# Performance work log

Measured on AMD Instinct MI355X. Metric: run time of the kernel, lower is better.

The kernel has to match this reference:

```python
import jax, jax.numpy as jnp
import numpy as np

DIM = 128
CODEBOOK_SIZE = 1024


def setup_inputs() -> dict:
    key = jax.random.key(0)
    kx, ke = jax.random.split(key)
    x = jax.random.normal(kx, (16, 4096, DIM), dtype=jnp.float32)
    # kaiming_uniform_ on (codebook_size, dim): bound = sqrt(6 / fan_in), fan_in = dim
    bound = float(np.sqrt(6.0 / DIM))
    embed = jax.random.uniform(ke, (CODEBOOK_SIZE, DIM), dtype=jnp.float32,
                               minval=-bound, maxval=bound)
    return {"x": x, "embed": embed}


def reference(x, embed):
    orig_shape = x.shape
    flat = x.reshape(-1, x.shape[-1])                     # [N, D]
    x2 = jnp.sum(flat * flat, axis=1, keepdims=True)      # [N, 1]
    e2 = jnp.sum(embed * embed, axis=1)                   # [K]
    dist = -(x2 - 2.0 * (flat @ embed.T) + e2[None, :])   # [N, K]
    embed_ind = jnp.argmax(dist, axis=-1)                 # [N]
    embed_ind = embed_ind.reshape(orig_shape[:-1])        # [B, S]
    quantize = jnp.take(embed, embed_ind, axis=0)         # [B, S, D]
    return quantize, embed_ind
```

## Files before the change

### kernel.cpp

```cpp
#include <hip/hip_runtime.h>

#define DIM     128
#define NCODES  1024
#define TILE_M  64
#define LDSS    136
#define DELTA   0.02f
#define RPB     4
#define RGRID   1024

typedef __attribute__((ext_vector_type(8))) _Float16 half8;
typedef __attribute__((ext_vector_type(4))) _Float16 half4;
typedef __attribute__((ext_vector_type(4))) float    f32x4;


__global__ __launch_bounds__(256) void prep_kernel(
    const float* __restrict__ embed, double* __restrict__ e2d,
    float* __restrict__ e2f, _Float16* __restrict__ eh, int* __restrict__ cnt)
{
  if (blockIdx.x == 0 && threadIdx.x == 0) *cnt = 0;
  const int w = threadIdx.x >> 6;
  const int l = threadIdx.x & 63;
  const int c = blockIdx.x * 4 + w;
  const float* row = embed + (size_t)c * DIM;
  float v0 = row[l], v1 = row[l + 64];
  eh[(size_t)c * DIM + l]      = (_Float16)v0;
  eh[(size_t)c * DIM + 64 + l] = (_Float16)v1;
  double sq = (double)v0 * v0 + (double)v1 * v1;
  #pragma unroll
  for (int off = 32; off >= 1; off >>= 1) sq += __shfl_down(sq, off, 64);
  if (l == 0) { e2d[c] = sq; e2f[c] = (float)sq; }
}

__global__ __launch_bounds__(256) void transpose_kernel(
    const float* __restrict__ embed, float* __restrict__ embedT)
{
  __shared__ float tile[64][65];
  const int c0 = blockIdx.y * 64;
  const int k0 = blockIdx.x * 64;
  const int t = threadIdx.x;
  #pragma unroll
  for (int i = 0; i < 16; ++i) {
    int idx = t + i * 256;
    int r = idx >> 6, c = idx & 63;
    tile[r][c] = embed[(size_t)(c0 + r) * DIM + k0 + c];
  }
  __syncthreads();
  #pragma unroll
  for (int i = 0; i < 16; ++i) {
    int idx = t + i * 256;
    int r = idx >> 6, c = idx & 63;
    embedT[(size_t)(k0 + r) * NCODES + c0 + c] = tile[c][r];
  }
}

__global__ __launch_bounds__(256, 2) void pass1_kernel(
    const float* __restrict__ x, const float* __restrict__ embed,
    const _Float16* __restrict__ eh, const float* __restrict__ e2f,
    float* __restrict__ outQ, float* __restrict__ outIdx,
    int* __restrict__ cnt, int* __restrict__ list)
{
  __shared__ _Float16 xh[TILE_M * LDSS];
  __shared__ float rb_best[4][TILE_M];
  __shared__ float rb_sec [4][TILE_M];
  __shared__ int   rb_idx [4][TILE_M];
  __shared__ int   fidx[TILE_M];

  const int tid  = threadIdx.x;
  const int row0 = blockIdx.x * TILE_M;

  {
    const f32x4* x4 = (const f32x4*)(x + (size_t)row0 * DIM);
    #pragma unroll
    for (int i = 0; i < 8; ++i) {
      int e = tid + i * 256;
      int r = e >> 5, c4 = e & 31;
      f32x4 v = x4[e];
      half4 h;
      h[0] = (_Float16)v[0]; h[1] = (_Float16)v[1];
      h[2] = (_Float16)v[2]; h[3] = (_Float16)v[3];
      *(half4*)&xh[r * LDSS + c4 * 4] = h;
    }
  }
  __syncthreads();

  const int l  = tid & 63, w = tid >> 6;
  const int rl = l & 15,  q = l >> 4;
  const int col0 = q * 8;

  half8 afrag[4][4];
  #pragma unroll
  for (int m = 0; m < 4; ++m)
    #pragma unroll
    for (int ks = 0; ks < 4; ++ks)
      afrag[m][ks] = *(const half8*)&xh[(m * 16 + rl) * LDSS + ks * 32 + col0];

  float bestv[16], secv[16]; int besti[16];
  #pragma unroll
  for (int s = 0; s < 16; ++s) { bestv[s] = 3.4e38f; secv[s] = 3.4e38f; besti[s] = 0; }

  const int codeBase = w * 256;

  half8 bcur[4], bnxt[4];
  {
    const half8* bb = (const half8*)(eh + (size_t)(codeBase + rl) * DIM + col0);
    #pragma unroll
    for (int ks = 0; ks < 4; ++ks) bcur[ks] = bb[ks * 4];
  }
  float e2cur = e2f[codeBase + rl];

  for (int ch = 0; ch < 16; ++ch) {
    const int mycode = codeBase + ch * 16 + rl;
    if (ch < 15) {
      const half8* bb = (const half8*)(eh + (size_t)(mycode + 16) * DIM + col0);
      #pragma unroll
      for (int ks = 0; ks < 4; ++ks) bnxt[ks] = bb[ks * 4];
    }
    float e2nxt = (ch < 15) ? e2f[mycode + 16] : 0.f;

    f32x4 acc[4];
    #pragma unroll
    for (int m = 0; m < 4; ++m) acc[m] = (f32x4){0.f, 0.f, 0.f, 0.f};
    #pragma unroll
    for (int ks = 0; ks < 4; ++ks)
      #pragma unroll
      for (int m = 0; m < 4; ++m)
        acc[m] = __builtin_amdgcn_mfma_f32_16x16x32_f16(afrag[m][ks], bcur[ks], acc[m], 0, 0, 0);

    #pragma unroll
    for (int m = 0; m < 4; ++m)
      #pragma unroll
      for (int r = 0; r < 4; ++r) {
        const int s = m * 4 + r;
        float sc = fmaf(-2.0f, acc[m][r], e2cur);
        secv[s]  = fminf(secv[s], fmaxf(bestv[s], sc));
        besti[s] = (sc < bestv[s]) ? mycode : besti[s];
        bestv[s] = fminf(bestv[s], sc);
      }

    #pragma unroll
    for (int ks = 0; ks < 4; ++ks) bcur[ks] = bnxt[ks];
    e2cur = e2nxt;
  }

  #pragma unroll
  for (int off = 1; off < 16; off <<= 1) {
    #pragma unroll
    for (int s = 0; s < 16; ++s) {
      float ob = __shfl_xor(bestv[s], off, 16);
      float os = __shfl_xor(secv[s],  off, 16);
      int   oi = __shfl_xor(besti[s], off, 16);
      bool take = (ob < bestv[s]) || (ob == bestv[s] && oi < besti[s]);
      float loser = take ? bestv[s] : ob;
      bestv[s] = take ? ob : bestv[s];
      besti[s] = take ? oi : besti[s];
      float m2 = os < loser ? os : loser;
      secv[s] = secv[s] < m2 ? secv[s] : m2;
    }
  }
  if (rl == 0) {
    #pragma unroll
    for (int m = 0; m < 4; ++m)
      #pragma unroll
      for (int r = 0; r < 4; ++r) {
        int s = m * 4 + r;
        int row = m * 16 + q * 4 + r;
        rb_best[w][row] = bestv[s];
        rb_sec [w][row] = secv[s];
        rb_idx [w][row] = besti[s];
      }
  }
  __syncthreads();

  if (tid < TILE_M) {
    float bv = rb_best[0][tid], sv = rb_sec[0][tid]; int bi = rb_idx[0][tid];
    #pragma unroll
    for (int ww = 1; ww < 4; ++ww) {
      float ob = rb_best[ww][tid], os = rb_sec[ww][tid]; int oi = rb_idx[ww][tid];
      bool take = (ob < bv) || (ob == bv && oi < bi);
      float loser = take ? bv : ob;
      bv = take ? ob : bv; bi = take ? oi : bi;
      float m2 = os < loser ? os : loser;
      sv = sv < m2 ? sv : m2;
    }
    int grow = row0 + tid;
    outIdx[grow] = (float)bi;
    fidx[tid] = bi;
    if (sv - bv <= DELTA) {
      int p = atomicAdd(cnt, 1);
      list[p] = grow;
    }
  }
  __syncthreads();

  {
    const f32x4* E4   = (const f32x4*)embed;
    f32x4*       out4 = (f32x4*)(outQ + (size_t)row0 * DIM);
    #pragma unroll
    for (int i = 0; i < 8; ++i) {
      int e = tid + i * 256;
      int r = e >> 5, c4 = e & 31;
      out4[e] = E4[fidx[r] * 32 + c4];
    }
  }
}

__global__ __launch_bounds__(256) void refine2_kernel(
    const float* __restrict__ x, const float* __restrict__ embed,
    const float* __restrict__ embedT,
    const double* __restrict__ e2d, const float* __restrict__ e2f,
    float* __restrict__ outQ, float* __restrict__ outIdx,
    const int* __restrict__ cnt, const int* __restrict__ list)
{
  __shared__ f32x4 xst[DIM];
  __shared__ float rb1[RPB][4], rb2[RPB][4];
  __shared__ int   ri1[RPB][4], ri2[RPB][4];
  __shared__ int   cand[RPB][2];

  const int t = threadIdx.x;
  const int l = t & 63, w = t >> 6;
  const int n = *cnt;
  float* xsf = (float*)xst;

  for (int base = blockIdx.x * RPB; base < n; base += RGRID * RPB) {
    const int nr = min(RPB, n - base);
    #pragma unroll
    for (int i = 0; i < 2; ++i) {
      int idx = t + i * 256;
      int r = idx >> 7, k = idx & 127;
      float v = 0.f;
      if (r < nr) v = x[(size_t)list[base + r] * DIM + k];
      xsf[k * RPB + r] = v;
    }
    __syncthreads();

    f32x4 dot[RPB];
    #pragma unroll
    for (int r = 0; r < RPB; ++r) dot[r] = (f32x4){0.f, 0.f, 0.f, 0.f};
    const f32x4* eT4 = (const f32x4*)embedT;
    #pragma unroll 4
    for (int k = 0; k < DIM; ++k) {
      f32x4 e4  = eT4[k * 256 + t];
      f32x4 xk4 = xst[k];
      #pragma unroll
      for (int r = 0; r < RPB; ++r) {
        dot[r][0] = fmaf(xk4[r], e4[0], dot[r][0]);
        dot[r][1] = fmaf(xk4[r], e4[1], dot[r][1]);
        dot[r][2] = fmaf(xk4[r], e4[2], dot[r][2]);
        dot[r][3] = fmaf(xk4[r], e4[3], dot[r][3]);
      }
    }

    #pragma unroll
    for (int r = 0; r < RPB; ++r) {
      float b1 = 3.4e38f, b2 = 3.4e38f; int i1 = 0, i2 = 0;
      #pragma unroll
      for (int j = 0; j < 4; ++j) {
        int c = 4 * t + j;
        float sc = fmaf(-2.0f, dot[r][j], e2f[c]);
        bool better = (sc < b1);
        float lv = better ? b1 : sc;  int li = better ? i1 : c;
        if (better) { b1 = sc; i1 = c; }
        bool t2 = (lv < b2) || (lv == b2 && li < i2);
        if (t2) { b2 = lv; i2 = li; }
      }
      #pragma unroll
      for (int off = 1; off < 64; off <<= 1) {
        float o1 = __shfl_xor(b1, off, 64); int oi1 = __shfl_xor(i1, off, 64);
        float o2 = __shfl_xor(b2, off, 64); int oi2 = __shfl_xor(i2, off, 64);
        bool take = (o1 < b1) || (o1 == b1 && oi1 < i1);
        float n1 = take ? o1 : b1; int ni1 = take ? oi1 : i1;
        float lo = take ? b1 : o1; int loi = take ? i1 : oi1;
        float c2v = take ? o2 : b2; int c2i = take ? oi2 : i2;
        bool u2 = (c2v < lo) || (c2v == lo && c2i < loi);
        b1 = n1; i1 = ni1;
        b2 = u2 ? c2v : lo; i2 = u2 ? c2i : loi;
      }
      if (l == 0) { rb1[r][w] = b1; ri1[r][w] = i1; rb2[r][w] = b2; ri2[r][w] = i2; }
    }
    __syncthreads();

    if (t < RPB) {
      float v1 = rb1[t][0], v2 = rb2[t][0]; int j1 = ri1[t][0], j2 = ri2[t][0];
      #pragma unroll
      for (int ww = 1; ww < 4; ++ww) {
        float o1 = rb1[t][ww], o2 = rb2[t][ww]; int oi1 = ri1[t][ww], oi2 = ri2[t][ww];
        bool take = (o1 < v1) || (o1 == v1 && oi1 < j1);
        float n1 = take ? o1 : v1; int ni1 = take ? oi1 : j1;
        float lo = take ? v1 : o1; int loi = take ? j1 : oi1;
        float c2v = take ? o2 : v2; int c2i = take ? oi2 : j2;
        bool u2 = (c2v < lo) || (c2v == lo && c2i < loi);
        v1 = n1; j1 = ni1; v2 = u2 ? c2v : lo; j2 = u2 ? c2i : loi;
      }
      cand[t][0] = j1; cand[t][1] = j2;
    }
    __syncthreads();

    if (w < nr) {
      int c1 = cand[w][0], c2 = cand[w][1];
      float xa = xsf[l * RPB + w], xb = xsf[(l + 64) * RPB + w];
      double p1 = (double)xa * (double)embed[(size_t)c1 * DIM + l]
                + (double)xb * (double)embed[(size_t)c1 * DIM + 64 + l];
      double p2 = (double)xa * (double)embed[(size_t)c2 * DIM + l]
                + (double)xb * (double)embed[(size_t)c2 * DIM + 64 + l];
      #pragma unroll
      for (int off = 1; off < 64; off <<= 1) {
        p1 += __shfl_xor(p1, off, 64);
        p2 += __shfl_xor(p2, off, 64);
      }
      double s1 = e2d[c1] - 2.0 * p1;
      double s2 = e2d[c2] - 2.0 * p2;
      int widx = ((s2 < s1) || (s2 == s1 && c2 < c1)) ? c2 : c1;
      int row = list[base + w];
      if (l == 0) outIdx[row] = (float)widx;
      outQ[(size_t)row * DIM + l]      = embed[(size_t)widx * DIM + l];
      outQ[(size_t)row * DIM + 64 + l] = embed[(size_t)widx * DIM + 64 + l];
    }
    __syncthreads();
  }
}

extern "C" void kernel_launch(void* const* d_in, const int* in_sizes, int n_in,
                              void* d_out, int out_size, void* d_ws, size_t ws_size,
                              hipStream_t stream) {
  const float* x     = (const float*)d_in[0];
  const float* embed = (const float*)d_in[1];
  const int N = in_sizes[0] / DIM;

  float* out    = (float*)d_out;
  float* outQ   = out;
  float* outIdx = out + (size_t)N * DIM;

  char* ws = (char*)d_ws;
  double*   e2d  = (double*)  (ws);
  float*    e2f  = (float*)   (ws + 8192);
  _Float16* eh   = (_Float16*)(ws + 12288);
  float*    eT   = (float*)   (ws + 274432);
  int*      cnt  = (int*)     (ws + 798720);
  int*      list = (int*)     (ws + 798976);

  prep_kernel     <<<NCODES / 4, 256, 0, stream>>>(embed, e2d, e2f, eh, cnt);
  dim3 tg(DIM / 64, NCODES / 64);
  transpose_kernel<<<tg,         256, 0, stream>>>(embed, eT);
  pass1_kernel    <<<N / TILE_M, 256, 0, stream>>>(x, embed, eh, e2f, outQ, outIdx, cnt, list);
  refine2_kernel  <<<RGRID,      256, 0, stream>>>(x, embed, eT, e2d, e2f, outQ, outIdx, cnt, list);
}
```

Before: 154.6 us.

## Pack code index into score mantissa and stream A fragments from LDS

The pass1 kernel now packs the code index into the low 10 mantissa bits of each distance score, so best/second tracking becomes plain fmin/fmax with no separate index registers or tie-break logic. A fragments are reloaded from LDS on every chunk instead of being held in 64 registers, and the B operand uses an explicit double buffer with unroll 2. The occupancy hint changes to four waves per EU. Together these cut register pressure and per-score ALU work. In exchange the score loses low mantissa bits, which the widened relative fallback threshold is meant to absorb, and LDS traffic goes up.

```diff
diff --git a/kernel.cpp b/kernel.cpp
--- a/kernel.cpp
+++ b/kernel.cpp
@@ -53,7 +53,9 @@
   }
 }
 
-__global__ __launch_bounds__(256, 2) void pass1_kernel(
+__global__ __launch_bounds__(256)
+__attribute__((amdgpu_waves_per_eu(4, 4)))
+void pass1_kernel(
     const float* __restrict__ x, const float* __restrict__ embed,
     const _Float16* __restrict__ eh, const float* __restrict__ e2f,
     float* __restrict__ outQ, float* __restrict__ outIdx,
@@ -62,7 +64,6 @@
   __shared__ _Float16 xh[TILE_M * LDSS];
   __shared__ float rb_best[4][TILE_M];
   __shared__ float rb_sec [4][TILE_M];
-  __shared__ int   rb_idx [4][TILE_M];
   __shared__ int   fidx[TILE_M];
 
   const int tid  = threadIdx.x;
@@ -86,75 +87,65 @@
   const int l  = tid & 63, w = tid >> 6;
   const int rl = l & 15,  q = l >> 4;
   const int col0 = q * 8;
-
-  half8 afrag[4][4];
-  #pragma unroll
-  for (int m = 0; m < 4; ++m)
-    #pragma unroll
-    for (int ks = 0; ks < 4; ++ks)
-      afrag[m][ks] = *(const half8*)&xh[(m * 16 + rl) * LDSS + ks * 32 + col0];
-
-  float bestv[16], secv[16]; int besti[16];
-  #pragma unroll
-  for (int s = 0; s < 16; ++s) { bestv[s] = 3.4e38f; secv[s] = 3.4e38f; besti[s] = 0; }
+  const int abase0 = rl * LDSS + col0;
+
+  float bestp[16], secp[16];
+  #pragma unroll
+  for (int s = 0; s < 16; ++s) { bestp[s] = 3.0e38f; secp[s] = 3.3e38f; }
 
   const int codeBase = w * 256;
-
-  half8 bcur[4], bnxt[4];
-  {
-    const half8* bb = (const half8*)(eh + (size_t)(codeBase + rl) * DIM + col0);
-    #pragma unroll
-    for (int ks = 0; ks < 4; ++ks) bcur[ks] = bb[ks * 4];
-  }
-  float e2cur = e2f[codeBase + rl];
-
+  const _Float16* ehw = eh + (size_t)(codeBase + rl) * DIM + col0;
+
+  half8 bbuf[2][4];
+  float e2buf[2];
+  #pragma unroll
+  for (int ks = 0; ks < 4; ++ks) bbuf[0][ks] = *(const half8*)(ehw + ks * 32);
+  e2buf[0] = e2f[codeBase + rl];
+
+  #pragma unroll 2
   for (int ch = 0; ch < 16; ++ch) {
+    const int cur = ch & 1, nxt = cur ^ 1;
     const int mycode = codeBase + ch * 16 + rl;
     if (ch < 15) {
-      const half8* bb = (const half8*)(eh + (size_t)(mycode + 16) * DIM + col0);
-      #pragma unroll
-      for (int ks = 0; ks < 4; ++ks) bnxt[ks] = bb[ks * 4];
-    }
-    float e2nxt = (ch < 15) ? e2f[mycode + 16] : 0.f;
-
-    f32x4 acc[4];
-    #pragma unroll
-    for (int m = 0; m < 4; ++m) acc[m] = (f32x4){0.f, 0.f, 0.f, 0.f};
-    #pragma unroll
-    for (int ks = 0; ks < 4; ++ks)
-      #pragma unroll
-      for (int m = 0; m < 4; ++m)
-        acc[m] = __builtin_amdgcn_mfma_f32_16x16x32_f16(afrag[m][ks], bcur[ks], acc[m], 0, 0, 0);
-
-    #pragma unroll
-    for (int m = 0; m < 4; ++m)
+      const _Float16* ehn = ehw + (size_t)(ch + 1) * (16 * DIM);
+      #pragma unroll
+      for (int ks = 0; ks < 4; ++ks) bbuf[nxt][ks] = *(const half8*)(ehn + ks * 32);
+      e2buf[nxt] = e2f[mycode + 16];
+    }
+    const float e2c = e2buf[cur];
+
+    int ozero = 0;
+    asm volatile("" : "+v"(ozero));
+    const int ab = abase0 + ozero;
+
+    #pragma unroll
+    for (int m = 0; m < 4; ++m) {
+      f32x4 acc = (f32x4){0.f, 0.f, 0.f, 0.f};
+      #pragma unroll
+      for (int ks = 0; ks < 4; ++ks) {
+        half8 af = *(const half8*)&xh[ab + m * (16 * LDSS) + ks * 32];
+        acc = __builtin_amdgcn_mfma_f32_16x16x32_f16(af, bbuf[cur][ks], acc, 0, 0, 0);
+      }
       #pragma unroll
       for (int r = 0; r < 4; ++r) {
         const int s = m * 4 + r;
-        float sc = fmaf(-2.0f, acc[m][r], e2cur);
-        secv[s]  = fminf(secv[s], fmaxf(bestv[s], sc));
-        besti[s] = (sc < bestv[s]) ? mycode : besti[s];
-        bestv[s] = fminf(bestv[s], sc);
-      }
-
-    #pragma unroll
-    for (int ks = 0; ks < 4; ++ks) bcur[ks] = bnxt[ks];
-    e2cur = e2nxt;
+        float sc  = fmaf(-2.0f, acc[r], e2c);
+        float scp = __int_as_float((__float_as_int(sc) & ~1023) | mycode);
+        secp[s]  = fminf(secp[s], fmaxf(bestp[s], scp));
+        bestp[s] = fminf(bestp[s], scp);
+      }
+    }
   }
 
   #pragma unroll
   for (int off = 1; off < 16; off <<= 1) {
     #pragma unroll
     for (int s = 0; s < 16; ++s) {
-      float ob = __shfl_xor(bestv[s], off, 16);
-      float os = __shfl_xor(secv[s],  off, 16);
-      int   oi = __shfl_xor(besti[s], off, 16);
-      bool take = (ob < bestv[s]) || (ob == bestv[s] && oi < besti[s]);
-      float loser = take ? bestv[s] : ob;
-      bestv[s] = take ? ob : bestv[s];
-      besti[s] = take ? oi : besti[s];
-      float m2 = os < loser ? os : loser;
-      secv[s] = secv[s] < m2 ? secv[s] : m2;
+      float ob = __shfl_xor(bestp[s], off, 16);
+      float os = __shfl_xor(secp[s],  off, 16);
+      float mx = fmaxf(bestp[s], ob);
+      bestp[s] = fminf(bestp[s], ob);
+      secp[s]  = fminf(fminf(secp[s], os), mx);
     }
   }
   if (rl == 0) {
@@ -164,28 +155,26 @@
       for (int r = 0; r < 4; ++r) {
         int s = m * 4 + r;
         int row = m * 16 + q * 4 + r;
-        rb_best[w][row] = bestv[s];
-        rb_sec [w][row] = secv[s];
-        rb_idx [w][row] = besti[s];
+        rb_best[w][row] = bestp[s];
+        rb_sec [w][row] = secp[s];
       }
   }
   __syncthreads();
 
   if (tid < TILE_M) {
-    float bv = rb_best[0][tid], sv = rb_sec[0][tid]; int bi = rb_idx[0][tid];
+    float bv = rb_best[0][tid], sv = rb_sec[0][tid];
     #pragma unroll
     for (int ww = 1; ww < 4; ++ww) {
-      float ob = rb_best[ww][tid], os = rb_sec[ww][tid]; int oi = rb_idx[ww][tid];
-      bool take = (ob < bv) || (ob == bv && oi < bi);
-      float loser = take ? bv : ob;
-      bv = take ? ob : bv; bi = take ? oi : bi;
-      float m2 = os < loser ? os : loser;
-      sv = sv < m2 ? sv : m2;
-    }
+      float ob = rb_best[ww][tid], os = rb_sec[ww][tid];
+      float mx = fmaxf(bv, ob);
+      bv = fminf(bv, ob);
+      sv = fminf(fminf(sv, os), mx);
+    }
+    int bi = __float_as_int(bv) & 1023;
     int grow = row0 + tid;
     outIdx[grow] = (float)bi;
     fidx[tid] = bi;
-    if (sv - bv <= DELTA) {
+    if (sv - bv <= DELTA + fabsf(bv) * 4.8828125e-4f) {
       int p = atomicAdd(cnt, 1);
       list[p] = grow;
     }
```

Result: faster. 141.5 us (-8.5%).
